# Kernel tuning notes

Measured on AMD Instinct MI355X. Metric: run time of the kernel, lower is better.

Reference implementation:

```python
import jax, jax.numpy as jnp
import numpy as np

N, E, DIN, DOUT, NNZ = 8192, 4096, 256, 128, 65536
TEMP = float(DOUT) ** 0.5
NEG = -1e9


def setup_inputs() -> dict:
    key = jax.random.key(0)
    ks = jax.random.split(key, 8)
    stdv = 1.0 / np.sqrt(DOUT)
    u = lambda k, shp: jax.random.uniform(k, shp, jnp.float32, -stdv, stdv)
    x = jax.random.normal(ks[0], (N, DIN), jnp.float32)
    nodes = jax.random.randint(ks[1], (NNZ,), 0, N, jnp.int32)
    edges = jax.random.randint(ks[2], (NNZ,), 0, E, jnp.int32)
    hyperedge_index = jnp.stack([nodes, edges])  # [2, nnz]
    return {
        "x": x,
        "weight": u(ks[3], (DIN, DOUT)),   # transfer weight
        "weight2": u(ks[4], (DIN, DOUT)),
        "weight3": u(ks[5], (DOUT, DOUT)),
        "bias": u(ks[6], (DOUT,)),
        "q_ctx": u(ks[7], (DOUT,)),        # word_context.weight[0]
        "hyperedge_index": hyperedge_index,
        "num_nodes": N,
        "num_edges": E,
    }


def reference(x, weight, weight2, weight3, bias, q_ctx, hyperedge_index, num_nodes, num_edges):
    # dense incidence H[node, edge] = 1  (hyperedge_preprocess)
    H = jnp.zeros((num_nodes, num_edges), x.dtype).at[
        hyperedge_index[0], hyperedge_index[1]].set(1.0)
    adj = H.T                       # [E, N]  (mask / original attention for attn1)

    x4 = x @ weight2                # [N, D]  x_4att
    xt = x @ weight + bias          # [N, D]  transferred features (v of attn1)

    # ---- attention1: query = shared word-context vector, keys = x4 ----
    row = (q_ctx / TEMP) @ x4.T                    # [N] (q1 rows are identical)
    scores1 = jnp.where(adj == 0, NEG, row[None, :])  # [E, N]
    att1 = jax.nn.softmax(adj, axis=-1) + jax.nn.softmax(scores1, axis=-1)
    edge = att1 @ xt                               # [E, D]

    att2he = att1.T                                # [N, E]

    # ---- attention2: queries = x4, keys = edge @ W3 ----
    edge4 = edge @ weight3                         # [E, D]
    scores2 = jnp.where(adj.T == 0, NEG, (x4 / TEMP) @ edge4.T)  # [N, E]
    att2hn = jax.nn.softmax(adj.T, axis=-1) + jax.nn.softmax(scores2, axis=-1)

    # ---- fused outer-product attention and output projection ----
    A = att2he @ att2he.T + att2hn @ att2hn.T      # [N, N]
    h_prime_g = jax.nn.elu(A @ x4)                 # [N, D]
    return h_prime_g
```

## Files before the change

kernel.cpp:

```cpp
#include <hip/hip_runtime.h>
#include <math.h>

constexpr int Nn   = 8192;
constexpr int Ee   = 4096;
constexpr int DIN  = 256;
constexpr int DOUT = 128;
constexpr int NNZ  = 65536;
constexpr int EC   = 96;
constexpr int NC   = 48;

#define TEMPR 0.08838834764831845f
#define EM1   1.7182818284590452f


typedef __attribute__((ext_vector_type(8))) short short8;
typedef __attribute__((ext_vector_type(4))) float f32x4;

static __device__ __forceinline__ float wave_sum64(float v) {
#pragma unroll
    for (int m = 32; m; m >>= 1) v += __shfl_xor(v, m, 64);
    return v;
}
static __device__ __forceinline__ float wave_max64(float v) {
#pragma unroll
    for (int m = 32; m; m >>= 1) v = fmaxf(v, __shfl_xor(v, m, 64));
    return v;
}
static __device__ __forceinline__ short f2bf(float f) {
    union { float f; unsigned u; } v; v.f = f;
    const unsigned r = (v.u + 0x7FFFu + ((v.u >> 16) & 1u)) >> 16;
    return (short)r;
}
static __device__ __forceinline__ unsigned packbf2(float a, float b) {
    return ((unsigned)(unsigned short)f2bf(a)) |
           (((unsigned)(unsigned short)f2bf(b)) << 16);
}
static __device__ __forceinline__ float2 unpackbf2(unsigned u) {
    union { unsigned u; float f; } lo, hi;
    lo.u = u << 16; hi.u = u & 0xFFFF0000u;
    return make_float2(lo.f, hi.f);
}

__global__ __launch_bounds__(256) void k_ww3(
    const float* __restrict__ W, const float* __restrict__ W2,
    const float* __restrict__ W3, const float* __restrict__ bias,
    short* __restrict__ W2T, short* __restrict__ WWT, float* __restrict__ bW3,
    uint4* __restrict__ zb, unsigned zTot16)
{
    const int b = blockIdx.x;
    const int t = threadIdx.x;
    if (b < 32) {
        __shared__ float sW[8][128];
        const int r0 = b * 8;
        for (int i = t; i < 1024; i += 256)
            sW[i >> 7][i & 127] = W[(size_t)(r0 + (i >> 7)) * DOUT + (i & 127)];
        __syncthreads();
        const int c  = t & 127;
        const int rh = (t >> 7) * 4;
        float acc[4] = {0.f, 0.f, 0.f, 0.f};
        for (int k = 0; k < 128; ++k) {
            const float w3 = W3[(size_t)k * DOUT + c];
#pragma unroll
            for (int i = 0; i < 4; ++i) acc[i] = fmaf(sW[rh + i][k], w3, acc[i]);
        }
#pragma unroll
        for (int i = 0; i < 4; ++i)
            WWT[(size_t)c * DIN + (r0 + rh + i)] = f2bf(acc[i]);
    } else if (b < 40) {
        const int k0 = (b - 32) * 32;
        for (int i = t; i < 32 * 128; i += 256) {
            const int k = k0 + (i >> 7);
            const int n = i & 127;
            W2T[(size_t)n * DIN + k] = f2bf(W2[(size_t)k * DOUT + n]);
        }
    } else if (b == 40) {
        if (t < 128) {
            float acc = 0.f;
            for (int k = 0; k < 128; ++k)
                acc = fmaf(bias[k], W3[(size_t)k * DOUT + t], acc);
            bW3[t] = acc;
        }
    } else {
        uint4 z; z.x = z.y = z.z = z.w = 0u;
        for (unsigned i = (unsigned)(b - 41) * 256u + t; i < zTot16;
             i += 64u * 256u)
            zb[i] = z;
    }
}

__global__ __launch_bounds__(256) void k_gemm1f(
    const float* __restrict__ x, const short* __restrict__ W2T,
    const short* __restrict__ WWT, const float* __restrict__ bW3,
    const float* __restrict__ q, const int* __restrict__ hidx,
    unsigned* __restrict__ bitmap, int* __restrict__ degE, int* __restrict__ degN,
    int* __restrict__ csrEn, int* __restrict__ csrNe, int* __restrict__ csrNs,
    unsigned* __restrict__ x4b, unsigned* __restrict__ xwb,
    float* __restrict__ rowv)
{
    __shared__ float srow[16];
    const int t    = threadIdx.x;
    const int lane = t & 63;
    const int wv   = t >> 6;
    const int n16  = lane & 15;
    const int quad = lane >> 4;
    const int r0   = blockIdx.x * 16;
    const int n0   = wv * 32;

    const unsigned gid = blockIdx.x * 256 + t;
    if (gid < NNZ) {
        const int n = hidx[gid];
        const int e = hidx[NNZ + gid];
        const unsigned word = (unsigned)n * (unsigned)Ee + (unsigned)e;
        const unsigned bit  = 1u << (word & 31u);
        const unsigned old  = atomicOr(&bitmap[word >> 5], bit);
        if (!(old & bit)) {
            const int pe = atomicAdd(&degE[e], 1);
            if (pe < EC) {
                csrEn[e * EC + pe] = n;
                const int pn = atomicAdd(&degN[n], 1);
                if (pn < NC) {
                    csrNe[n * NC + pn] = e;
                    csrNs[n * NC + pn] = e * EC + pe;
                }
            }
        }
    }

    f32x4 acc4[2], accw[2];
#pragma unroll
    for (int nt = 0; nt < 2; ++nt) {
        acc4[nt] = (f32x4){0.f, 0.f, 0.f, 0.f};
        accw[nt] = (f32x4){0.f, 0.f, 0.f, 0.f};
    }
#pragma unroll
    for (int k0 = 0; k0 < DIN; k0 += 32) {
        const int kb = k0 + quad * 8;
        const float4 xa = *(const float4*)&x[(size_t)(r0 + n16) * DIN + kb];
        const float4 xb = *(const float4*)&x[(size_t)(r0 + n16) * DIN + kb + 4];
        short8 af;
        af[0] = f2bf(xa.x); af[1] = f2bf(xa.y); af[2] = f2bf(xa.z); af[3] = f2bf(xa.w);
        af[4] = f2bf(xb.x); af[5] = f2bf(xb.y); af[6] = f2bf(xb.z); af[7] = f2bf(xb.w);
#pragma unroll
        for (int nt = 0; nt < 2; ++nt) {
            const int col = n0 + nt * 16 + n16;
            const short8 b4 = *(const short8*)&W2T[(size_t)col * DIN + kb];
            const short8 bw = *(const short8*)&WWT[(size_t)col * DIN + kb];
            acc4[nt] = __builtin_amdgcn_mfma_f32_16x16x32_bf16(af, b4, acc4[nt], 0, 0, 0);
            accw[nt] = __builtin_amdgcn_mfma_f32_16x16x32_bf16(af, bw, accw[nt], 0, 0, 0);
        }
    }

    float bwv[2], qv[2];
#pragma unroll
    for (int nt = 0; nt < 2; ++nt) {
        const int col = n0 + nt * 16 + n16;
        bwv[nt] = bW3[col];
        qv[nt]  = q[col];
    }
    const int s = wv * 16 + n16;
#pragma unroll
    for (int reg = 0; reg < 4; ++reg) {
        const int row = r0 + quad * 4 + reg;
        x4b[(size_t)row * 64 + s] = packbf2(acc4[0][reg], acc4[1][reg]);
        xwb[(size_t)row * 64 + s] = packbf2(accw[0][reg] + bwv[0],
                                            accw[1][reg] + bwv[1]);
    }
    float pr[4];
#pragma unroll
    for (int reg = 0; reg < 4; ++reg)
        pr[reg] = qv[0] * acc4[0][reg] + qv[1] * acc4[1][reg];
#pragma unroll
    for (int m = 8; m; m >>= 1) {
#pragma unroll
        for (int reg = 0; reg < 4; ++reg) pr[reg] += __shfl_xor(pr[reg], m, 64);
    }
    if (t < 16) srow[t] = 0.f;
    __syncthreads();
    if (n16 == 0) {
#pragma unroll
        for (int reg = 0; reg < 4; ++reg) atomicAdd(&srow[quad * 4 + reg], pr[reg]);
    }
    __syncthreads();
    if (t < 16) rowv[r0 + t] = srow[t] * TEMPR;
}

__global__ __launch_bounds__(256) void k_reduxA(
    const unsigned* __restrict__ x4b, const unsigned* __restrict__ xwb,
    const int* __restrict__ degE,
    float* __restrict__ csx4, float* __restrict__ csxw, float* __restrict__ c2g)
{
    const int t    = threadIdx.x;
    const int lane = t & 63;
    const int w    = t >> 6;
    const int b    = blockIdx.x;
    float2 a4 = {0.f, 0.f}, aw = {0.f, 0.f};
    for (int k = 0; k < 32; ++k) {
        const int n = b * 128 + w + k * 4;
        const float2 fv = unpackbf2(x4b[(size_t)n * 64 + lane]);
        const float2 tv = unpackbf2(xwb[(size_t)n * 64 + lane]);
        a4.x += fv.x; a4.y += fv.y;
        aw.x += tv.x; aw.y += tv.y;
    }
    atomicAdd(&csx4[lane * 2 + 0], a4.x); atomicAdd(&csx4[lane * 2 + 1], a4.y);
    atomicAdd(&csxw[lane * 2 + 0], aw.x); atomicAdd(&csxw[lane * 2 + 1], aw.y);

    const int gid = b * 256 + t;
    if (gid < Ee) {
        const int de = min(degE[gid], EC);
        const float ue = de ? 1.0f / ((float)Nn + (float)de * EM1)
                            : 2.0f / (float)Nn;
        const float v = wave_sum64(ue * ue);
        if (lane == 0) atomicAdd(c2g, v);
    }
}

__global__ __launch_bounds__(128, 4) void k_edge1(
    const int* __restrict__ degE, const int* __restrict__ csrEn,
    const float* __restrict__ rowv,
    const float* __restrict__ csx4, const float* __restrict__ csxw,
    const unsigned* __restrict__ x4b, const unsigned* __restrict__ xwb,
    float* __restrict__ Sval, unsigned* __restrict__ e4b, unsigned* __restrict__ G1b,
    float* __restrict__ wsArr)
{
    __shared__ int   sN[2][EC];
    __shared__ float sS[2][EC];
    const int t    = threadIdx.x;
    const int w    = t >> 6;
    const int lane = t & 63;
    const int e    = blockIdx.x * 2 + w;
    const int deg  = min(degE[e], EC);
    const float ue = deg ? 1.0f / ((float)Nn + (float)deg * EM1) : 2.0f / (float)Nn;

    int   n0 = 0, n1 = 0;
    float r0 = -INFINITY, r1 = -INFINITY;
    if (lane < deg)      { n0 = csrEn[e * EC + lane];      r0 = rowv[n0]; }
    if (lane + 64 < deg) { n1 = csrEn[e * EC + lane + 64]; r1 = rowv[n1]; }
    const float m  = wave_max64(fmaxf(r0, r1));
    const float e0 = (lane < deg)      ? expf(r0 - m) : 0.f;
    const float e1 = (lane + 64 < deg) ? expf(r1 - m) : 0.f;
    const float Z  = wave_sum64(e0 + e1);
    const float inv = deg ? 1.0f / Z : 0.f;
    const float base = EM1 * ue;
    if (lane < deg) {
        const float sv = fmaf(e0, inv, base);
        sN[w][lane] = n0; sS[w][lane] = sv;
        Sval[e * EC + lane] = sv;
        atomicAdd(&wsArr[n0], ue * sv);
    }
    if (lane + 64 < deg) {
        const float sv = fmaf(e1, inv, base);
        sN[w][lane + 64] = n1; sS[w][lane + 64] = sv;
        Sval[e * EC + lane + 64] = sv;
        atomicAdd(&wsArr[n1], ue * sv);
    }

    const float2 cw = *(const float2*)&csxw[lane * 2];
    const float2 c4 = *(const float2*)&csx4[lane * 2];
    float2 aE = make_float2(ue * cw.x, ue * cw.y);
    float2 aG = make_float2(ue * c4.x, ue * c4.y);
    int j = 0;
    for (; j + 16 <= deg; j += 16) {
        int ai[16]; float bi[16]; unsigned tu[16], fu[16];
#pragma unroll
        for (int k = 0; k < 16; ++k) { ai[k] = sN[w][j+k]; bi[k] = sS[w][j+k]; }
#pragma unroll
        for (int k = 0; k < 16; ++k) {
            tu[k] = xwb[(size_t)ai[k] * 64 + lane];
            fu[k] = x4b[(size_t)ai[k] * 64 + lane];
        }
#pragma unroll
        for (int k = 0; k < 16; ++k) {
            const float2 tv = unpackbf2(tu[k]);
            const float2 fv = unpackbf2(fu[k]);
            aE.x = fmaf(bi[k], tv.x, aE.x); aE.y = fmaf(bi[k], tv.y, aE.y);
            aG.x = fmaf(bi[k], fv.x, aG.x); aG.y = fmaf(bi[k], fv.y, aG.y);
        }
    }
    for (; j + 8 <= deg; j += 8) {
        int ai[8]; float bi[8]; unsigned tu[8], fu[8];
#pragma unroll
        for (int k = 0; k < 8; ++k) { ai[k] = sN[w][j+k]; bi[k] = sS[w][j+k]; }
#pragma unroll
        for (int k = 0; k < 8; ++k) {
            tu[k] = xwb[(size_t)ai[k] * 64 + lane];
            fu[k] = x4b[(size_t)ai[k] * 64 + lane];
        }
#pragma unroll
        for (int k = 0; k < 8; ++k) {
            const float2 tv = unpackbf2(tu[k]);
            const float2 fv = unpackbf2(fu[k]);
            aE.x = fmaf(bi[k], tv.x, aE.x); aE.y = fmaf(bi[k], tv.y, aE.y);
            aG.x = fmaf(bi[k], fv.x, aG.x); aG.y = fmaf(bi[k], fv.y, aG.y);
        }
    }
    for (; j < deg; ++j) {
        const int   a = sN[w][j];
        const float b = sS[w][j];
        const float2 tv = unpackbf2(xwb[(size_t)a * 64 + lane]);
        const float2 fv = unpackbf2(x4b[(size_t)a * 64 + lane]);
        aE.x = fmaf(b, tv.x, aE.x); aE.y = fmaf(b, tv.y, aE.y);
        aG.x = fmaf(b, fv.x, aG.x); aG.y = fmaf(b, fv.y, aG.y);
    }
    e4b[(size_t)e * 64 + lane] = packbf2(aE.x, aE.y);
    G1b[(size_t)e * 64 + lane] = packbf2(aG.x, aG.y);
}

__global__ __launch_bounds__(256) void k_nodeB(
    const int* __restrict__ degN, const int* __restrict__ csrNe,
    const int* __restrict__ csrNs, const unsigned* __restrict__ x4b,
    const unsigned* __restrict__ e4b, const float* __restrict__ wsArr,
    float* __restrict__ Tval,
    float* __restrict__ vxg, float* __restrict__ twg, float* __restrict__ wsg)
{
    const int t    = threadIdx.x;
    const int w    = t >> 6;
    const int lane = t & 63;
    const int b    = blockIdx.x;

    if (b < 64) {
        float2 av = {0.f, 0.f}, at2 = {0.f, 0.f}, aw = {0.f, 0.f};
        for (int k = 0; k < 32; ++k) {
            const int n   = b * 128 + w + k * 4;
            const int deg = min(degN[n], NC);
            const float vn = deg ? 1.0f / ((float)Ee + (float)deg * EM1)
                                 : 2.0f / (float)Ee;
            const float tw = deg ? fmaf((float)deg * EM1, vn, 1.0f) : 0.f;
            const float wsn = wsArr[n];
            const float2 xv = unpackbf2(x4b[(size_t)n * 64 + lane]);
            av.x  = fmaf(vn,  xv.x, av.x);  av.y  = fmaf(vn,  xv.y, av.y);
            at2.x = fmaf(tw,  xv.x, at2.x); at2.y = fmaf(tw,  xv.y, at2.y);
            aw.x  = fmaf(wsn, xv.x, aw.x);  aw.y  = fmaf(wsn, xv.y, aw.y);
        }
        atomicAdd(&vxg[lane*2+0], av.x);  atomicAdd(&vxg[lane*2+1], av.y);
        atomicAdd(&twg[lane*2+0], at2.x); atomicAdd(&twg[lane*2+1], at2.y);
        atomicAdd(&wsg[lane*2+0], aw.x);  atomicAdd(&wsg[lane*2+1], aw.y);
        return;
    }

    const int es   = lane >> 3;
    const int dl   = lane & 7;
    const int n    = (b - 64) * 4 + w;
    const int deg  = min(degN[n], NC);
    if (!deg) return;
    const float vn = 1.0f / ((float)Ee + (float)deg * EM1);

    const uint4* xr = (const uint4*)&x4b[(size_t)n * 64];
    const uint4 xua = xr[dl * 2], xub = xr[dl * 2 + 1];
    const float2 x0 = unpackbf2(xua.x), x1 = unpackbf2(xua.y),
                 x2 = unpackbf2(xua.z), x3 = unpackbf2(xua.w),
                 x4v = unpackbf2(xub.x), x5 = unpackbf2(xub.y),
                 x6 = unpackbf2(xub.z), x7 = unpackbf2(xub.w);

    float dps[6]; float exs[6]; int slots[6];
    float m = -INFINITY;
#pragma unroll
    for (int p = 0; p < 6; ++p) {
        dps[p] = -INFINITY; slots[p] = 0;
        if (p * 8 >= deg) continue;
        const int j = p * 8 + es;
        int ej = 0;
        if (j < deg) { ej = csrNe[n * NC + j]; slots[p] = csrNs[n * NC + j]; }
        const uint4* er = (const uint4*)&e4b[(size_t)ej * 64];
        const uint4 ea = er[dl * 2], eb = er[dl * 2 + 1];
        float d0 = 0.f, d1 = 0.f, d2 = 0.f, d3 = 0.f;
        { const float2 ev = unpackbf2(ea.x); d0 = fmaf(ev.x, x0.x, d0); d0 = fmaf(ev.y, x0.y, d0); }
        { const float2 ev = unpackbf2(ea.y); d1 = fmaf(ev.x, x1.x, d1); d1 = fmaf(ev.y, x1.y, d1); }
        { const float2 ev = unpackbf2(ea.z); d2 = fmaf(ev.x, x2.x, d2); d2 = fmaf(ev.y, x2.y, d2); }
        { const float2 ev = unpackbf2(ea.w); d3 = fmaf(ev.x, x3.x, d3); d3 = fmaf(ev.y, x3.y, d3); }
        { const float2 ev = unpackbf2(eb.x); d0 = fmaf(ev.x, x4v.x, d0); d0 = fmaf(ev.y, x4v.y, d0); }
        { const float2 ev = unpackbf2(eb.y); d1 = fmaf(ev.x, x5.x, d1); d1 = fmaf(ev.y, x5.y, d1); }
        { const float2 ev = unpackbf2(eb.z); d2 = fmaf(ev.x, x6.x, d2); d2 = fmaf(ev.y, x6.y, d2); }
        { const float2 ev = unpackbf2(eb.w); d3 = fmaf(ev.x, x7.x, d3); d3 = fmaf(ev.y, x7.y, d3); }
        float dot = (d0 + d1) + (d2 + d3);
        dot += __shfl_xor(dot, 1, 64);
        dot += __shfl_xor(dot, 2, 64);
        dot += __shfl_xor(dot, 4, 64);
        dot = (j < deg) ? dot * TEMPR : -INFINITY;
        dps[p] = dot;
        float mm = fmaxf(dot, __shfl_xor(dot, 8, 64));
        mm = fmaxf(mm, __shfl_xor(mm, 16, 64));
        mm = fmaxf(mm, __shfl_xor(mm, 32, 64));
        m = fmaxf(m, mm);
    }
    float Z = 0.f;
#pragma unroll
    for (int p = 0; p < 6; ++p) {
        exs[p] = 0.f;
        if (p * 8 >= deg) continue;
        const float ex = (p * 8 + es < deg) ? expf(dps[p] - m) : 0.f;
        exs[p] = ex;
        float sum = ex + __shfl_xor(ex, 8, 64);
        sum += __shfl_xor(sum, 16, 64);
        sum += __shfl_xor(sum, 32, 64);
        Z += sum;
    }
    const float invZ = 1.0f / Z;
#pragma unroll
    for (int p = 0; p < 6; ++p) {
        if (p * 8 >= deg) continue;
        if (dl == 0 && p * 8 + es < deg)
            Tval[slots[p]] = fmaf(EM1, vn, exs[p] * invZ);
    }
}

__global__ __launch_bounds__(128, 4) void k_g2(
    const int* __restrict__ degE, const int* __restrict__ csrEn,
    const float* __restrict__ Tval, const float* __restrict__ vxg,
    const unsigned* __restrict__ x4b, unsigned* __restrict__ G2b)
{
    const int t    = threadIdx.x;
    const int w    = t >> 6;
    const int lane = t & 63;
    const int e    = blockIdx.x * 2 + w;
    const int deg  = min(degE[e], EC);
    float2 acc = *(const float2*)&vxg[lane * 2];
    int j = 0;
    for (; j + 16 <= deg; j += 16) {
        int ai[16]; float bi[16]; unsigned fu[16];
#pragma unroll
        for (int k = 0; k < 16; ++k) { ai[k] = csrEn[e*EC+j+k]; bi[k] = Tval[e*EC+j+k]; }
#pragma unroll
        for (int k = 0; k < 16; ++k)
            fu[k] = x4b[(size_t)ai[k] * 64 + lane];
#pragma unroll
        for (int k = 0; k < 16; ++k) {
            const float2 fv = unpackbf2(fu[k]);
            acc.x = fmaf(bi[k], fv.x, acc.x); acc.y = fmaf(bi[k], fv.y, acc.y);
        }
    }
    for (; j + 8 <= deg; j += 8) {
        int ai[8]; float bi[8]; unsigned fu[8];
#pragma unroll
        for (int k = 0; k < 8; ++k) { ai[k] = csrEn[e*EC+j+k]; bi[k] = Tval[e*EC+j+k]; }
#pragma unroll
        for (int k = 0; k < 8; ++k)
            fu[k] = x4b[(size_t)ai[k] * 64 + lane];
#pragma unroll
        for (int k = 0; k < 8; ++k) {
            const float2 fv = unpackbf2(fu[k]);
            acc.x = fmaf(bi[k], fv.x, acc.x); acc.y = fmaf(bi[k], fv.y, acc.y);
        }
    }
    for (; j < deg; ++j) {
        const int   a = csrEn[e*EC+j];
        const float b = Tval[e*EC+j];
        const float2 fv = unpackbf2(x4b[(size_t)a * 64 + lane]);
        acc.x = fmaf(b, fv.x, acc.x); acc.y = fmaf(b, fv.y, acc.y);
    }
    G2b[(size_t)e * 64 + lane] = packbf2(acc.x, acc.y);
}

__global__ __launch_bounds__(128, 4) void k_final(
    const int* __restrict__ degN, const int* __restrict__ csrNe,
    const int* __restrict__ csrNs, const float* __restrict__ Sval,
    const float* __restrict__ Tval,
    const float* __restrict__ c2g, const float* __restrict__ csx4,
    const float* __restrict__ wsg, const float* __restrict__ vxg,
    const float* __restrict__ twg,
    const unsigned* __restrict__ G1b, const unsigned* __restrict__ G2b,
    float* __restrict__ out)
{
    const int t    = threadIdx.x;
    const int w    = t >> 6;
    const int lane = t & 63;
    const int n    = blockIdx.x * 2 + w;
    const int deg  = min(degN[n], NC);
    const float vn = deg ? 1.0f / ((float)Ee + (float)deg * EM1) : 2.0f / (float)Ee;
    const float c2 = *c2g;
    const float2 c4v = *(const float2*)&csx4[lane * 2];
    const float2 wsv = *(const float2*)&wsg[lane * 2];
    const float2 vxv = *(const float2*)&vxg[lane * 2];
    const float2 twv = *(const float2*)&twg[lane * 2];
    float2 acc;
    acc.x = fmaf(c2, c4v.x, wsv.x) + vn * fmaf((float)Ee, vxv.x, twv.x);
    acc.y = fmaf(c2, c4v.y, wsv.y) + vn * fmaf((float)Ee, vxv.y, twv.y);
    int j = 0;
    for (; j + 8 <= deg; j += 8) {
        int ei[8], si[8]; float sv[8], tv[8]; unsigned g1u[8], g2u[8];
#pragma unroll
        for (int k = 0; k < 8; ++k) {
            ei[k] = csrNe[n*NC+j+k]; si[k] = csrNs[n*NC+j+k];
        }
#pragma unroll
        for (int k = 0; k < 8; ++k) {
            sv[k] = Sval[si[k]]; tv[k] = Tval[si[k]];
            g1u[k] = G1b[(size_t)ei[k] * 64 + lane];
            g2u[k] = G2b[(size_t)ei[k] * 64 + lane];
        }
#pragma unroll
        for (int k = 0; k < 8; ++k) {
            const float2 g1 = unpackbf2(g1u[k]);
            const float2 g2 = unpackbf2(g2u[k]);
            acc.x = fmaf(sv[k], g1.x, acc.x); acc.y = fmaf(sv[k], g1.y, acc.y);
            acc.x = fmaf(tv[k], g2.x, acc.x); acc.y = fmaf(tv[k], g2.y, acc.y);
        }
    }
    for (; j + 4 <= deg; j += 4) {
        int ei[4], si[4]; float sv[4], tv[4]; unsigned g1u[4], g2u[4];
#pragma unroll
        for (int k = 0; k < 4; ++k) {
            ei[k] = csrNe[n*NC+j+k]; si[k] = csrNs[n*NC+j+k];
        }
#pragma unroll
        for (int k = 0; k < 4; ++k) {
            sv[k] = Sval[si[k]]; tv[k] = Tval[si[k]];
            g1u[k] = G1b[(size_t)ei[k] * 64 + lane];
            g2u[k] = G2b[(size_t)ei[k] * 64 + lane];
        }
#pragma unroll
        for (int k = 0; k < 4; ++k) {
            const float2 g1 = unpackbf2(g1u[k]);
            const float2 g2 = unpackbf2(g2u[k]);
            acc.x = fmaf(sv[k], g1.x, acc.x); acc.y = fmaf(sv[k], g1.y, acc.y);
            acc.x = fmaf(tv[k], g2.x, acc.x); acc.y = fmaf(tv[k], g2.y, acc.y);
        }
    }
    for (; j < deg; ++j) {
        const int ea = csrNe[n*NC+j];
        const int sa = csrNs[n*NC+j];
        const float sva = Sval[sa], tva = Tval[sa];
        const float2 g1a = unpackbf2(G1b[(size_t)ea * 64 + lane]);
        const float2 g2a = unpackbf2(G2b[(size_t)ea * 64 + lane]);
        acc.x = fmaf(sva, g1a.x, acc.x); acc.y = fmaf(sva, g1a.y, acc.y);
        acc.x = fmaf(tva, g2a.x, acc.x); acc.y = fmaf(tva, g2a.y, acc.y);
    }
    acc.x = acc.x > 0.f ? acc.x : expm1f(acc.x);
    acc.y = acc.y > 0.f ? acc.y : expm1f(acc.y);
    const int lo = ((lane >> 4) << 5) + (lane & 15);
    out[(size_t)n * DOUT + lo]      = acc.x;
    out[(size_t)n * DOUT + lo + 16] = acc.y;
}

extern "C" void kernel_launch(void* const* d_in, const int* in_sizes, int n_in,
                              void* d_out, int out_size, void* d_ws, size_t ws_size,
                              hipStream_t stream)
{
    const float* x    = (const float*)d_in[0];
    const float* W    = (const float*)d_in[1];
    const float* W2   = (const float*)d_in[2];
    const float* W3   = (const float*)d_in[3];
    const float* bias = (const float*)d_in[4];
    const float* q    = (const float*)d_in[5];
    const int*   hidx = (const int*)d_in[6];
    float* out = (float*)d_out;

    char* wsp = (char*)d_ws;
    size_t o = 0;
    auto take = [&](size_t bytes) {
        size_t r = o; o += (bytes + 255) & ~(size_t)255; return r;
    };
    unsigned* bitmap = (unsigned*)(wsp + take((size_t)Nn * Ee / 8));
    int*   degE  = (int*)  (wsp + take((size_t)Ee * 4));
    int*   degN  = (int*)  (wsp + take((size_t)Nn * 4));
    float* wsArr = (float*)(wsp + take((size_t)Nn * 4));
    float* c2g   = (float*)(wsp + take(4));
    float* csx4  = (float*)(wsp + take(DOUT * 4));
    float* csxw  = (float*)(wsp + take(DOUT * 4));
    float* vxg   = (float*)(wsp + take(DOUT * 4));
    float* twg   = (float*)(wsp + take(DOUT * 4));
    float* wsg   = (float*)(wsp + take(DOUT * 4));
    const size_t zbytes = o;
    unsigned* x4b   = (unsigned*)(wsp + take((size_t)Nn * 64 * 4));
    unsigned* xwb   = (unsigned*)(wsp + take((size_t)Nn * 64 * 4));
    float*    rowv  = (float*)   (wsp + take((size_t)Nn * 4));
    int*      csrEn = (int*)     (wsp + take((size_t)Ee * EC * 4));
    float*    Sval  = (float*)   (wsp + take((size_t)Ee * EC * 4));
    float*    Tval  = (float*)   (wsp + take((size_t)Ee * EC * 4));
    int*      csrNe = (int*)     (wsp + take((size_t)Nn * NC * 4));
    int*      csrNs = (int*)     (wsp + take((size_t)Nn * NC * 4));
    unsigned* e4b   = (unsigned*)(wsp + take((size_t)Ee * 64 * 4));
    unsigned* G1b   = (unsigned*)(wsp + take((size_t)Ee * 64 * 4));
    unsigned* G2b   = (unsigned*)(wsp + take((size_t)Ee * 64 * 4));
    short*    W2T   = (short*)   (wsp + take((size_t)DOUT * DIN * 2));
    short*    WWT   = (short*)   (wsp + take((size_t)DOUT * DIN * 2));
    float*    bW3   = (float*)   (wsp + take(DOUT * 4));
    (void)ws_size; (void)in_sizes; (void)n_in; (void)out_size;

    k_ww3   <<<105,       256, 0, stream>>>(W, W2, W3, bias, W2T, WWT, bW3,
                                            (uint4*)d_ws, (unsigned)(zbytes / 16));
    k_gemm1f<<<Nn / 16,   256, 0, stream>>>(x, W2T, WWT, bW3, q, hidx,
                                            bitmap, degE, degN, csrEn, csrNe, csrNs,
                                            x4b, xwb, rowv);
    k_reduxA<<<64,        256, 0, stream>>>(x4b, xwb, degE, csx4, csxw, c2g);
    k_edge1 <<<Ee / 2,    128, 0, stream>>>(degE, csrEn, rowv, csx4, csxw,
                                            x4b, xwb, Sval, e4b, G1b, wsArr);
    k_nodeB <<<64 + Nn/4, 256, 0, stream>>>(degN, csrNe, csrNs, x4b, e4b, wsArr,
                                            Tval, vxg, twg, wsg);
    k_g2    <<<Ee / 2,    128, 0, stream>>>(degE, csrEn, Tval, vxg, x4b, G2b);
    k_final <<<Nn / 2,    128, 0, stream>>>(degN, csrNe, csrNs, Sval, Tval,
                                            c2g, csx4, wsg, vxg, twg, G1b, G2b, out);
}
```

Before: 164.4 us.

## Compute column sums from x via linearity and drop the k_reduxA launch

The column sums of x4 and xt are now computed algebraically: k_ww3's zeroing blocks produce partial column sums of x, and an extra block in k_gemm1f multiplies the total by the bf16 weight matrices and adds Nn*bias·W3. The c2g degree reduction moves into k_nodeB's spare blocks. This removes one kernel launch and its re-read of the bf16 x4/xw buffers. The trade-off is an extra read of x in k_ww3 and a serial 256-length dot product in one block, and the sums now come from unrounded x rather than the bf16 products.

```diff
diff --git a/kernel.cpp b/kernel.cpp
--- a/kernel.cpp
+++ b/kernel.cpp
@@ -40,17 +40,25 @@
     lo.u = u << 16; hi.u = u & 0xFFFF0000u;
     return make_float2(lo.f, hi.f);
 }
+static __device__ __forceinline__ float bf2f(short s) {
+    union { unsigned u; float f; } v;
+    v.u = ((unsigned)(unsigned short)s) << 16;
+    return v.f;
+}
 
 __global__ __launch_bounds__(256) void k_ww3(
+    const float* __restrict__ x,
     const float* __restrict__ W, const float* __restrict__ W2,
     const float* __restrict__ W3, const float* __restrict__ bias,
     short* __restrict__ W2T, short* __restrict__ WWT, float* __restrict__ bW3,
+    float* __restrict__ sxPart,
     uint4* __restrict__ zb, unsigned zTot16)
 {
+    __shared__ float sW[8][128];
+    __shared__ float sxl[256];
     const int b = blockIdx.x;
     const int t = threadIdx.x;
     if (b < 32) {
-        __shared__ float sW[8][128];
         const int r0 = b * 8;
         for (int i = t; i < 1024; i += 256)
             sW[i >> 7][i & 127] = W[(size_t)(r0 + (i >> 7)) * DOUT + (i & 127)];
@@ -81,10 +89,27 @@
             bW3[t] = acc;
         }
     } else {
+        const int zb0 = b - 41;
         uint4 z; z.x = z.y = z.z = z.w = 0u;
-        for (unsigned i = (unsigned)(b - 41) * 256u + t; i < zTot16;
+        for (unsigned i = (unsigned)zb0 * 256u + t; i < zTot16;
              i += 64u * 256u)
             zb[i] = z;
+        const int lane = t & 63;
+        const int wv   = t >> 6;
+        float a0 = 0.f, a1 = 0.f, a2 = 0.f, a3 = 0.f;
+        for (int r = 0; r < 32; ++r) {
+            const int row = zb0 * 128 + wv * 32 + r;
+            const float4 v = *(const float4*)&x[(size_t)row * DIN + lane * 4];
+            a0 += v.x; a1 += v.y; a2 += v.z; a3 += v.w;
+        }
+        sxl[t] = 0.f;
+        __syncthreads();
+        atomicAdd(&sxl[lane * 4 + 0], a0);
+        atomicAdd(&sxl[lane * 4 + 1], a1);
+        atomicAdd(&sxl[lane * 4 + 2], a2);
+        atomicAdd(&sxl[lane * 4 + 3], a3);
+        __syncthreads();
+        sxPart[zb0 * 256 + t] = sxl[t];
     }
 }
 
@@ -92,13 +117,38 @@
     const float* __restrict__ x, const short* __restrict__ W2T,
     const short* __restrict__ WWT, const float* __restrict__ bW3,
     const float* __restrict__ q, const int* __restrict__ hidx,
+    const float* __restrict__ sxPart,
     unsigned* __restrict__ bitmap, int* __restrict__ degE, int* __restrict__ degN,
     int* __restrict__ csrEn, int* __restrict__ csrNe, int* __restrict__ csrNs,
     unsigned* __restrict__ x4b, unsigned* __restrict__ xwb,
-    float* __restrict__ rowv)
+    float* __restrict__ rowv, float* __restrict__ csx4, float* __restrict__ csxw)
 {
     __shared__ float srow[16];
-    const int t    = threadIdx.x;
+    __shared__ float sxv[256];
+    const int t = threadIdx.x;
+
+    if (blockIdx.x == 512) {
+        float s = 0.f;
+        for (int b2 = 0; b2 < 64; ++b2) s += sxPart[b2 * 256 + t];
+        sxv[t] = s;
+        __syncthreads();
+        const int c  = t & 127;
+        const int g  = c >> 5, r = c & 31;
+        const int pos = 2 * (g * 16 + (r & 15)) + (r >> 4);
+        if (t < 128) {
+            float acc = 0.f;
+            for (int k = 0; k < 256; ++k)
+                acc = fmaf(sxv[k], bf2f(W2T[(size_t)c * DIN + k]), acc);
+            csx4[pos] = acc;
+        } else {
+            float acc = 0.f;
+            for (int k = 0; k < 256; ++k)
+                acc = fmaf(sxv[k], bf2f(WWT[(size_t)c * DIN + k]), acc);
+            csxw[pos] = acc + (float)Nn * bW3[c];
+        }
+        return;
+    }
+
     const int lane = t & 63;
     const int wv   = t >> 6;
     const int n16  = lane & 15;
@@ -184,36 +234,6 @@
     if (t < 16) rowv[r0 + t] = srow[t] * TEMPR;
 }
 
-__global__ __launch_bounds__(256) void k_reduxA(
-    const unsigned* __restrict__ x4b, const unsigned* __restrict__ xwb,
-    const int* __restrict__ degE,
-    float* __restrict__ csx4, float* __restrict__ csxw, float* __restrict__ c2g)
-{
-    const int t    = threadIdx.x;
-    const int lane = t & 63;
-    const int w    = t >> 6;
-    const int b    = blockIdx.x;
-    float2 a4 = {0.f, 0.f}, aw = {0.f, 0.f};
-    for (int k = 0; k < 32; ++k) {
-        const int n = b * 128 + w + k * 4;
-        const float2 fv = unpackbf2(x4b[(size_t)n * 64 + lane]);
-        const float2 tv = unpackbf2(xwb[(size_t)n * 64 + lane]);
-        a4.x += fv.x; a4.y += fv.y;
-        aw.x += tv.x; aw.y += tv.y;
-    }
-    atomicAdd(&csx4[lane * 2 + 0], a4.x); atomicAdd(&csx4[lane * 2 + 1], a4.y);
-    atomicAdd(&csxw[lane * 2 + 0], aw.x); atomicAdd(&csxw[lane * 2 + 1], aw.y);
-
-    const int gid = b * 256 + t;
-    if (gid < Ee) {
-        const int de = min(degE[gid], EC);
-        const float ue = de ? 1.0f / ((float)Nn + (float)de * EM1)
-                            : 2.0f / (float)Nn;
-        const float v = wave_sum64(ue * ue);
-        if (lane == 0) atomicAdd(c2g, v);
-    }
-}
-
 __global__ __launch_bounds__(128, 4) void k_edge1(
     const int* __restrict__ degE, const int* __restrict__ csrEn,
     const float* __restrict__ rowv,
@@ -306,11 +326,13 @@
 }
 
 __global__ __launch_bounds__(256) void k_nodeB(
-    const int* __restrict__ degN, const int* __restrict__ csrNe,
+    const int* __restrict__ degN, const int* __restrict__ degE,
+    const int* __restrict__ csrNe,
     const int* __restrict__ csrNs, const unsigned* __restrict__ x4b,
     const unsigned* __restrict__ e4b, const float* __restrict__ wsArr,
     float* __restrict__ Tval,
-    float* __restrict__ vxg, float* __restrict__ twg, float* __restrict__ wsg)
+    float* __restrict__ vxg, float* __restrict__ twg, float* __restrict__ wsg,
+    float* __restrict__ c2g)
 {
     const int t    = threadIdx.x;
     const int w    = t >> 6;
@@ -334,6 +356,14 @@
         atomicAdd(&vxg[lane*2+0], av.x);  atomicAdd(&vxg[lane*2+1], av.y);
         atomicAdd(&twg[lane*2+0], at2.x); atomicAdd(&twg[lane*2+1], at2.y);
         atomicAdd(&wsg[lane*2+0], aw.x);  atomicAdd(&wsg[lane*2+1], aw.y);
+        const int gid = b * 256 + t;
+        if (gid < Ee) {
+            const int de = min(degE[gid], EC);
+            const float ue = de ? 1.0f / ((float)Nn + (float)de * EM1)
+                                : 2.0f / (float)Nn;
+            const float v = wave_sum64(ue * ue);
+            if (lane == 0) atomicAdd(c2g, v);
+        }
         return;
     }
 
@@ -554,12 +584,13 @@
     int*   degN  = (int*)  (wsp + take((size_t)Nn * 4));
     float* wsArr = (float*)(wsp + take((size_t)Nn * 4));
     float* c2g   = (float*)(wsp + take(4));
-    float* csx4  = (float*)(wsp + take(DOUT * 4));
-    float* csxw  = (float*)(wsp + take(DOUT * 4));
     float* vxg   = (float*)(wsp + take(DOUT * 4));
     float* twg   = (float*)(wsp + take(DOUT * 4));
     float* wsg   = (float*)(wsp + take(DOUT * 4));
     const size_t zbytes = o;
+    float*    csx4  = (float*)   (wsp + take(DOUT * 4));
+    float*    csxw  = (float*)   (wsp + take(DOUT * 4));
+    float*    sxPart= (float*)   (wsp + take(64 * 256 * 4));
     unsigned* x4b   = (unsigned*)(wsp + take((size_t)Nn * 64 * 4));
     unsigned* xwb   = (unsigned*)(wsp + take((size_t)Nn * 64 * 4));
     float*    rowv  = (float*)   (wsp + take((size_t)Nn * 4));
@@ -576,16 +607,16 @@
     float*    bW3   = (float*)   (wsp + take(DOUT * 4));
     (void)ws_size; (void)in_sizes; (void)n_in; (void)out_size;
 
-    k_ww3   <<<105,       256, 0, stream>>>(W, W2, W3, bias, W2T, WWT, bW3,
-                                            (uint4*)d_ws, (unsigned)(zbytes / 16));
-    k_gemm1f<<<Nn / 16,   256, 0, stream>>>(x, W2T, WWT, bW3, q, hidx,
+    k_ww3   <<<105,       256, 0, stream>>>(x, W, W2, W3, bias, W2T, WWT, bW3,
+                                            sxPart, (uint4*)d_ws,
+                                            (unsigned)(zbytes / 16));
+    k_gemm1f<<<513,       256, 0, stream>>>(x, W2T, WWT, bW3, q, hidx, sxPart,
                                             bitmap, degE, degN, csrEn, csrNe, csrNs,
-                                            x4b, xwb, rowv);
-    k_reduxA<<<64,        256, 0, stream>>>(x4b, xwb, degE, csx4, csxw, c2g);
+                                            x4b, xwb, rowv, csx4, csxw);
     k_edge1 <<<Ee / 2,    128, 0, stream>>>(degE, csrEn, rowv, csx4, csxw,
                                             x4b, xwb, Sval, e4b, G1b, wsArr);
-    k_nodeB <<<64 + Nn/4, 256, 0, stream>>>(degN, csrNe, csrNs, x4b, e4b, wsArr,
-                                            Tval, vxg, twg, wsg);
+    k_nodeB <<<64 + Nn/4, 256, 0, stream>>>(degN, degE, csrNe, csrNs, x4b, e4b,
+                                            wsArr, Tval, vxg, twg, wsg, c2g);
     k_g2    <<<Ee / 2,    128, 0, stream>>>(degE, csrEn, Tval, vxg, x4b, G2b);
     k_final <<<Nn / 2,    128, 0, stream>>>(degN, csrNe, csrNs, Sval, Tval,
                                             c2g, csx4, wsg, vxg, twg, G1b, G2b, out);
```

New measurement: 154.7 us. -5.9%, faster.
